# Optimization experiments

Hardware: AMD Instinct MI355X
Metric: run time of the kernel (lower is better)

Reference implementation:

```python
import jax, jax.numpy as jnp
import numpy as np

H = 256          # h_dim
SEQ_LEN = 10     # max history length
B = 2048         # number of queries with non-empty history
N = 327680       # total flattened neighbors across all (query, timestep) segments
NUM_SEG = B * SEQ_LEN
NUM_ENT = 20000
NUM_REL = 200


def setup_inputs() -> dict:
    key = jax.random.key(0)
    ks = jax.random.split(key, 9)
    s = jax.random.randint(ks[0], (B,), 0, NUM_ENT)
    r = jax.random.randint(ks[1], (B,), 0, NUM_REL)
    nbr_ids = jax.random.randint(ks[2], (N,), 0, NUM_ENT)
    seg_ids = jnp.sort(jax.random.randint(ks[3], (N,), 0, NUM_SEG))
    ent_embeds = jax.random.normal(ks[4], (NUM_ENT, H), dtype=jnp.float32)
    rel_embeds = jax.random.normal(ks[5], (NUM_REL, H), dtype=jnp.float32)
    W_attn = jax.random.normal(ks[6], (3 * H, H), dtype=jnp.float32) * 0.05
    b_attn = jax.random.normal(ks[7], (H,), dtype=jnp.float32) * 0.05
    v_s = jax.random.normal(ks[8], (H, 1), dtype=jnp.float32) * 0.05
    return {"s": s, "r": r, "nbr_ids": nbr_ids, "seg_ids": seg_ids,
            "ent_embeds": ent_embeds, "rel_embeds": rel_embeds,
            "W_attn": W_attn, "b_attn": b_attn, "v_s": v_s}


def reference(s, r, nbr_ids, seg_ids, ent_embeds, rel_embeds, W_attn, b_attn, v_s):
    # Per-neighbor gathers. Each neighbor belongs to segment seg = q*SEQ_LEN + t.
    q = seg_ids // SEQ_LEN                              # query index per neighbor [N]
    em = ent_embeds[nbr_ids]                            # [N, H] neighbor embeddings
    s_emb = ent_embeds[s]                               # [B, H]
    r_emb = rel_embeds[r]                               # [B, H]
    ss = s_emb[q]                                       # [N, H]
    rr = r_emb[q]                                       # [N, H]
    # Score: tanh(Linear(3H -> H)) @ v_s  -> scalar per neighbor
    x = jnp.concatenate([em, ss, rr], axis=1)           # [N, 3H]
    scores = (jnp.tanh(x @ W_attn + b_attn) @ v_s)[:, 0]  # [N]
    # Segment softmax over neighbors within each (query, timestep) segment.
    m = jax.ops.segment_max(scores, seg_ids, num_segments=NUM_SEG)  # [S]
    e = jnp.exp(scores - m[seg_ids])                    # [N]
    denom = jax.ops.segment_sum(e, seg_ids, num_segments=NUM_SEG)   # [S]
    w = e / denom[seg_ids]                              # [N]
    # Weighted sum of neighbor embeddings per segment (scatter-reduce).
    agg = jax.ops.segment_sum(w[:, None] * em, seg_ids, num_segments=NUM_SEG)  # [S, H]
    counts = jax.ops.segment_sum(jnp.ones_like(scores), seg_ids, num_segments=NUM_SEG)
    mask = (counts > 0).astype(em.dtype).reshape(B, SEQ_LEN, 1)     # present timesteps
    agg = agg.reshape(B, SEQ_LEN, H)
    ss_t = jnp.broadcast_to(s_emb[:, None, :], (B, SEQ_LEN, H))
    rr_t = jnp.broadcast_to(r_emb[:, None, :], (B, SEQ_LEN, H))
    # Padded [B, SEQ_LEN, 3H] sequence tensor (rows for empty segments are zero,
    # matching the torch code's zero-initialized padded tensor). Dropout p=0.0.
    out = jnp.concatenate([agg, ss_t, rr_t], axis=2) * mask
    return out
```

## Files before the change

kernel.cpp:

```cpp
#include <hip/hip_runtime.h>
#include <hip/hip_bf16.h>

#define H 256
#define SEQ 10
#define C2LOG2E 2.8853900817779268f
#define LOG2E 1.4426950408889634f

typedef __attribute__((ext_vector_type(8))) short bf16x8;
typedef __attribute__((ext_vector_type(4))) float f32x4;

__device__ __forceinline__ unsigned short f2bf(float x) {
    union { float f; unsigned u; } v; v.f = x;
    unsigned r = v.u + 0x7fff + ((v.u >> 16) & 1);
    return (unsigned short)(r >> 16);
}
__device__ __forceinline__ float bf2f(unsigned short b) {
    union { unsigned u; float f; } v; v.u = ((unsigned)b) << 16;
    return v.f;
}
__device__ __forceinline__ float fexp2(float x) {
    return __builtin_amdgcn_exp2f(x);
}

__global__ void prep_kernel(const float* __restrict__ W,
                            unsigned short* __restrict__ Wt,
                            const int* __restrict__ seg_ids,
                            int* __restrict__ seg_start,
                            int nWt, int n, int num_seg) {
    if ((int)blockIdx.x < nWt) {
        int idx = blockIdx.x * 256 + threadIdx.x;
        if (idx >= H * 3 * H) return;
        int nn = idx / (3 * H), k = idx % (3 * H);
        Wt[idx] = f2bf(C2LOG2E * W[k * H + nn]);
    } else {
        int j = (blockIdx.x - nWt) * 256 + threadIdx.x;
        if (j >= n) return;
        int cur = seg_ids[j];
        int prev = (j == 0) ? -1 : seg_ids[j - 1];
        for (int s2 = prev + 1; s2 <= cur; s2++) seg_start[s2] = j;
        if (j == n - 1)
            for (int s2 = cur + 1; s2 <= num_seg; s2++) seg_start[s2] = n;
    }
}

__global__ void gemm_bf16_kernel(const float* __restrict__ entf,
                                 const int* __restrict__ sidx,
                                 const int* __restrict__ ridx,
                                 const float* __restrict__ ent,
                                 const float* __restrict__ rel,
                                 const unsigned short* __restrict__ Wt,
                                 const float* __restrict__ bias,
                                 unsigned short* __restrict__ out,
                                 unsigned short* __restrict__ em_out,
                                 int M, int K, int k0, int mode, int ldo) {
    __shared__ unsigned short As[64][40];
    __shared__ unsigned short Bs[256][40];
    int t = threadIdx.x;
    int m0 = blockIdx.x * 64;
    int sr = t >> 2;
    int sc = (t & 3) * 8;
    int wave = t >> 6, lane = t & 63;
    int lr = lane & 15, lg = lane >> 4;

    f32x4 acc[4][4];
#pragma unroll
    for (int i = 0; i < 4; i++)
#pragma unroll
        for (int jn = 0; jn < 4; jn++) acc[i][jn] = (f32x4){0.f, 0.f, 0.f, 0.f};

    for (int kk = 0; kk < K; kk += 32) {
        bf16x8 av = {};
        int gm = m0 + sr;
        if (gm < M) {
            const float* src;
            if (mode == 0) {
                src = entf + (size_t)gm * H + kk + sc;
            } else {
                int k = kk + sc;
                src = (k < H) ? (ent + (size_t)sidx[gm] * H + k)
                              : (rel + (size_t)ridx[gm] * H + (k - H));
            }
            float4 f0 = *reinterpret_cast<const float4*>(src);
            float4 f1 = *reinterpret_cast<const float4*>(src + 4);
            av[0] = (short)f2bf(f0.x); av[1] = (short)f2bf(f0.y);
            av[2] = (short)f2bf(f0.z); av[3] = (short)f2bf(f0.w);
            av[4] = (short)f2bf(f1.x); av[5] = (short)f2bf(f1.y);
            av[6] = (short)f2bf(f1.z); av[7] = (short)f2bf(f1.w);
            if (mode == 0 && em_out)
                *reinterpret_cast<bf16x8*>(em_out + (size_t)gm * 512 + 256 + kk + sc) = av;
        }
        *reinterpret_cast<bf16x8*>(&As[sr][sc]) = av;
#pragma unroll
        for (int r4 = 0; r4 < 4; r4++) {
            int row = r4 * 64 + sr;
            bf16x8 bv = *reinterpret_cast<const bf16x8*>(
                Wt + (size_t)row * (3 * H) + k0 + kk + sc);
            *reinterpret_cast<bf16x8*>(&Bs[row][sc]) = bv;
        }
        __syncthreads();

        bf16x8 afr[4], bfr[4];
#pragma unroll
        for (int am = 0; am < 4; am++)
            afr[am] = *reinterpret_cast<const bf16x8*>(&As[am * 16 + lr][lg * 8]);
#pragma unroll
        for (int bn = 0; bn < 4; bn++)
            bfr[bn] = *reinterpret_cast<const bf16x8*>(&Bs[wave * 64 + bn * 16 + lr][lg * 8]);
#pragma unroll
        for (int am = 0; am < 4; am++)
#pragma unroll
            for (int bn = 0; bn < 4; bn++)
                acc[am][bn] = __builtin_amdgcn_mfma_f32_16x16x32_bf16(
                    afr[am], bfr[bn], acc[am][bn], 0, 0, 0);
        __syncthreads();
    }

#pragma unroll
    for (int bn = 0; bn < 4; bn++) {
        int col = wave * 64 + bn * 16 + lr;
        float bv = bias ? C2LOG2E * bias[col] : 0.f;
#pragma unroll
        for (int am = 0; am < 4; am++) {
#pragma unroll
            for (int rr = 0; rr < 4; rr++) {
                int row = m0 + am * 16 + lg * 4 + rr;
                if (row < M)
                    out[(size_t)row * ldo + col] = f2bf(acc[am][bn][rr] + bv);
            }
        }
    }
}

__global__ void __launch_bounds__(128, 4)
fused_agg_kernel(const int* __restrict__ nbr_ids,
                 const int* __restrict__ seg_start,
                 const unsigned short* __restrict__ comb,
                 const unsigned short* __restrict__ qpartbf,
                 const float* __restrict__ v_s,
                 const float* __restrict__ ent_embeds,
                 const float* __restrict__ rel_embeds,
                 const int* __restrict__ s,
                 const int* __restrict__ r,
                 float* __restrict__ out, int num_seg) {
    int wid = blockIdx.x * 2 + (threadIdx.x >> 6);
    int nw = gridDim.x * 2;
    int lane = threadIdx.x & 63;
    int g = lane >> 4, li = lane & 15;
    int cb = li * 16;
    int c4 = lane * 4;

    int chunk = (num_seg + nw - 1) / nw;
    int sbeg = wid * chunk;
    int send = min(sbeg + chunk, num_seg);

    float vm2[16];
    float vsum = 0.f;
    {
        const float4* vp = reinterpret_cast<const float4*>(v_s + cb);
#pragma unroll
        for (int k = 0; k < 4; k++) {
            float4 tv = vp[k];
            vm2[4 * k + 0] = -2.f * tv.x; vm2[4 * k + 1] = -2.f * tv.y;
            vm2[4 * k + 2] = -2.f * tv.z; vm2[4 * k + 3] = -2.f * tv.w;
            vsum += tv.x + tv.y + tv.z + tv.w;
        }
    }

    float qv[16];
    int bcur = -1;

    for (int seg = sbeg; seg < send; seg++) {
        int start = seg_start[seg], end = seg_start[seg + 1];
        int b = seg / SEQ;
        float* orow = out + (size_t)seg * (3 * H);

        if (start == end) {
            float4 z = {0.f, 0.f, 0.f, 0.f};
            *reinterpret_cast<float4*>(orow + c4) = z;
            *reinterpret_cast<float4*>(orow + H + c4) = z;
            *reinterpret_cast<float4*>(orow + 2 * H + c4) = z;
            continue;
        }

        if (b != bcur) {
            bcur = b;
            bf16x8 qa = *reinterpret_cast<const bf16x8*>(qpartbf + (size_t)b * H + cb);
            bf16x8 qb = *reinterpret_cast<const bf16x8*>(qpartbf + (size_t)b * H + cb + 8);
#pragma unroll
            for (int k = 0; k < 8; k++) {
                qv[k] = bf2f((unsigned short)qa[k]);
                qv[8 + k] = bf2f((unsigned short)qb[k]);
            }
        }

        float acc[16];
#pragma unroll
        for (int k = 0; k < 16; k++) acc[k] = 0.f;
        float lpart = 0.f;

        int cc = end - start;
        int nitm = (cc + 3) >> 2;

        int j0 = min(g, cc - 1);
        const unsigned short* row = comb + (size_t)nbr_ids[start + j0] * 512 + cb;
        bf16x8 p0 = *reinterpret_cast<const bf16x8*>(row);
        bf16x8 p1 = *reinterpret_cast<const bf16x8*>(row + 8);

        for (int ji = 0; ji < nitm; ji++) {
            bf16x8 e0 = *reinterpret_cast<const bf16x8*>(row + 256);
            bf16x8 e1 = *reinterpret_cast<const bf16x8*>(row + 264);
            int jn = min(4 * (ji + 1) + g, cc - 1);
            const unsigned short* rown = comb + (size_t)nbr_ids[start + jn] * 512 + cb;
            bf16x8 p0n = *reinterpret_cast<const bf16x8*>(rown);
            bf16x8 p1n = *reinterpret_cast<const bf16x8*>(rown + 8);

            float s16 = 0.f;
#pragma unroll
            for (int k = 0; k < 8; k++) {
                float r0 = __builtin_amdgcn_rcpf(
                    fexp2(bf2f((unsigned short)p0[k]) + qv[k]) + 1.f);
                s16 = fmaf(vm2[k], r0, s16);
                float r1 = __builtin_amdgcn_rcpf(
                    fexp2(bf2f((unsigned short)p1[k]) + qv[8 + k]) + 1.f);
                s16 = fmaf(vm2[8 + k], r1, s16);
            }
            s16 += vsum;
            s16 += __shfl_xor(s16, 1);
            s16 += __shfl_xor(s16, 2);
            s16 += __shfl_xor(s16, 4);
            s16 += __shfl_xor(s16, 8);
            float e = fexp2(s16 * LOG2E);
            e = (4 * ji + g < cc) ? e : 0.f;
            lpart += e;
#pragma unroll
            for (int k = 0; k < 8; k++) {
                acc[k] = fmaf(e, bf2f((unsigned short)e0[k]), acc[k]);
                acc[8 + k] = fmaf(e, bf2f((unsigned short)e1[k]), acc[8 + k]);
            }
            p0 = p0n; p1 = p1n; row = rown;
        }

        lpart += __shfl_xor(lpart, 16);
        lpart += __shfl_xor(lpart, 32);
#pragma unroll
        for (int k = 0; k < 16; k++) {
            acc[k] += __shfl_xor(acc[k], 16);
            acc[k] += __shfl_xor(acc[k], 32);
        }
        float invl = 1.f / lpart;

        float4 o;
#pragma unroll
        for (int k = 0; k < 4; k++) {
            float v0 = acc[k], v1 = acc[4 + k], v2 = acc[8 + k], v3 = acc[12 + k];
            float pick = (g == 0) ? v0 : (g == 1) ? v1 : (g == 2) ? v2 : v3;
            if (k == 0) o.x = pick * invl;
            else if (k == 1) o.y = pick * invl;
            else if (k == 2) o.z = pick * invl;
            else o.w = pick * invl;
        }
        *reinterpret_cast<float4*>(orow + cb + 4 * g) = o;
        *reinterpret_cast<float4*>(orow + H + c4) =
            *reinterpret_cast<const float4*>(ent_embeds + (size_t)s[b] * H + c4);
        *reinterpret_cast<float4*>(orow + 2 * H + c4) =
            *reinterpret_cast<const float4*>(rel_embeds + (size_t)r[b] * H + c4);
    }
}

extern "C" void kernel_launch(void* const* d_in, const int* in_sizes, int n_in,
                              void* d_out, int out_size, void* d_ws, size_t ws_size,
                              hipStream_t stream) {
    const int* s = (const int*)d_in[0];
    const int* r = (const int*)d_in[1];
    const int* nbr_ids = (const int*)d_in[2];
    const int* seg_ids = (const int*)d_in[3];
    const float* ent_embeds = (const float*)d_in[4];
    const float* rel_embeds = (const float*)d_in[5];
    const float* W_attn = (const float*)d_in[6];
    const float* b_attn = (const float*)d_in[7];
    const float* v_s = (const float*)d_in[8];
    float* out = (float*)d_out;

    int B = in_sizes[0];
    int N = in_sizes[2];
    int num_ent = in_sizes[4] / H;
    int num_seg = B * SEQ;

    char* ws = (char*)d_ws;
    unsigned short* comb = (unsigned short*)ws;
    unsigned short* Wt = comb + (size_t)num_ent * 512;
    unsigned short* qpartbf = Wt + (size_t)H * 3 * H;
    int* seg_start = (int*)(qpartbf + (size_t)B * H);

    int nWt = (H * 3 * H + 255) / 256;
    int nSeg = (N + 255) / 256;
    prep_kernel<<<nWt + nSeg, 256, 0, stream>>>(W_attn, Wt, seg_ids, seg_start,
                                                nWt, N, num_seg);

    gemm_bf16_kernel<<<(num_ent + 63) / 64, 256, 0, stream>>>(
        ent_embeds, nullptr, nullptr, nullptr, nullptr,
        Wt, nullptr, comb, comb, num_ent, H, 0, 0, 512);
    gemm_bf16_kernel<<<B / 64, 256, 0, stream>>>(
        nullptr, s, r, ent_embeds, rel_embeds,
        Wt, b_attn, qpartbf, nullptr, B, 2 * H, H, 1, H);

    fused_agg_kernel<<<2048, 128, 0, stream>>>(
        nbr_ids, seg_start, comb, qpartbf, v_s,
        ent_embeds, rel_embeds, s, r, out, num_seg);
}
```

Measured before the change: 106.0 us.

## Use atomic work-stealing for segment aggregation and merge the two GEMM launches

Static per-wave segment chunks in the aggregation kernel are replaced by dynamic work distribution, where each wave atomically grabs two segments from a global counter. This is meant to balance the uneven neighbor counts across segments. The entity-projection and query-projection GEMMs are merged into a single launch by splitting on block index, removing one kernel launch and letting the small query GEMM overlap with the larger one. Block size and launch bounds for the aggregation kernel also go up. The cost is atomic contention on one counter, and the counter has to be reset inside the prep kernel.

```diff
diff --git a/kernel.cpp b/kernel.cpp
--- a/kernel.cpp
+++ b/kernel.cpp
@@ -26,7 +26,9 @@
                             unsigned short* __restrict__ Wt,
                             const int* __restrict__ seg_ids,
                             int* __restrict__ seg_start,
+                            int* __restrict__ work_ctr,
                             int nWt, int n, int num_seg) {
+    if (blockIdx.x == 0 && threadIdx.x == 0) *work_ctr = 0;
     if ((int)blockIdx.x < nWt) {
         int idx = blockIdx.x * 256 + threadIdx.x;
         if (idx >= H * 3 * H) return;
@@ -46,17 +48,23 @@
 __global__ void gemm_bf16_kernel(const float* __restrict__ entf,
                                  const int* __restrict__ sidx,
                                  const int* __restrict__ ridx,
-                                 const float* __restrict__ ent,
                                  const float* __restrict__ rel,
                                  const unsigned short* __restrict__ Wt,
                                  const float* __restrict__ bias,
-                                 unsigned short* __restrict__ out,
-                                 unsigned short* __restrict__ em_out,
-                                 int M, int K, int k0, int mode, int ldo) {
+                                 unsigned short* __restrict__ comb,
+                                 unsigned short* __restrict__ qpart,
+                                 int nEntBlk, int M0, int M1) {
     __shared__ unsigned short As[64][40];
     __shared__ unsigned short Bs[256][40];
+    bool isEnt = (int)blockIdx.x < nEntBlk;
+    int m0 = (isEnt ? blockIdx.x : (blockIdx.x - nEntBlk)) * 64;
+    int M = isEnt ? M0 : M1;
+    int K = isEnt ? H : 2 * H;
+    int k0 = isEnt ? 0 : H;
+    int ldo = isEnt ? 512 : H;
+    unsigned short* outp = isEnt ? comb : qpart;
+
     int t = threadIdx.x;
-    int m0 = blockIdx.x * 64;
     int sr = t >> 2;
     int sc = (t & 3) * 8;
     int wave = t >> 6, lane = t & 63;
@@ -73,11 +81,11 @@
         int gm = m0 + sr;
         if (gm < M) {
             const float* src;
-            if (mode == 0) {
+            if (isEnt) {
                 src = entf + (size_t)gm * H + kk + sc;
             } else {
                 int k = kk + sc;
-                src = (k < H) ? (ent + (size_t)sidx[gm] * H + k)
+                src = (k < H) ? (entf + (size_t)sidx[gm] * H + k)
                               : (rel + (size_t)ridx[gm] * H + (k - H));
             }
             float4 f0 = *reinterpret_cast<const float4*>(src);
@@ -86,8 +94,8 @@
             av[2] = (short)f2bf(f0.z); av[3] = (short)f2bf(f0.w);
             av[4] = (short)f2bf(f1.x); av[5] = (short)f2bf(f1.y);
             av[6] = (short)f2bf(f1.z); av[7] = (short)f2bf(f1.w);
-            if (mode == 0 && em_out)
-                *reinterpret_cast<bf16x8*>(em_out + (size_t)gm * 512 + 256 + kk + sc) = av;
+            if (isEnt)
+                *reinterpret_cast<bf16x8*>(comb + (size_t)gm * 512 + 256 + kk + sc) = av;
         }
         *reinterpret_cast<bf16x8*>(&As[sr][sc]) = av;
 #pragma unroll
@@ -118,20 +126,20 @@
 #pragma unroll
     for (int bn = 0; bn < 4; bn++) {
         int col = wave * 64 + bn * 16 + lr;
-        float bv = bias ? C2LOG2E * bias[col] : 0.f;
+        float bv = isEnt ? 0.f : C2LOG2E * bias[col];
 #pragma unroll
         for (int am = 0; am < 4; am++) {
 #pragma unroll
             for (int rr = 0; rr < 4; rr++) {
                 int row = m0 + am * 16 + lg * 4 + rr;
                 if (row < M)
-                    out[(size_t)row * ldo + col] = f2bf(acc[am][bn][rr] + bv);
-            }
-        }
-    }
-}
-
-__global__ void __launch_bounds__(128, 4)
+                    outp[(size_t)row * ldo + col] = f2bf(acc[am][bn][rr] + bv);
+            }
+        }
+    }
+}
+
+__global__ void __launch_bounds__(256, 6)
 fused_agg_kernel(const int* __restrict__ nbr_ids,
                  const int* __restrict__ seg_start,
                  const unsigned short* __restrict__ comb,
@@ -141,17 +149,12 @@
                  const float* __restrict__ rel_embeds,
                  const int* __restrict__ s,
                  const int* __restrict__ r,
+                 int* __restrict__ work_ctr,
                  float* __restrict__ out, int num_seg) {
-    int wid = blockIdx.x * 2 + (threadIdx.x >> 6);
-    int nw = gridDim.x * 2;
     int lane = threadIdx.x & 63;
     int g = lane >> 4, li = lane & 15;
     int cb = li * 16;
     int c4 = lane * 4;
-
-    int chunk = (num_seg + nw - 1) / nw;
-    int sbeg = wid * chunk;
-    int send = min(sbeg + chunk, num_seg);
 
     float vm2[16];
     float vsum = 0.f;
@@ -169,101 +172,109 @@
     float qv[16];
     int bcur = -1;
 
-    for (int seg = sbeg; seg < send; seg++) {
-        int start = seg_start[seg], end = seg_start[seg + 1];
-        int b = seg / SEQ;
-        float* orow = out + (size_t)seg * (3 * H);
-
-        if (start == end) {
-            float4 z = {0.f, 0.f, 0.f, 0.f};
-            *reinterpret_cast<float4*>(orow + c4) = z;
-            *reinterpret_cast<float4*>(orow + H + c4) = z;
-            *reinterpret_cast<float4*>(orow + 2 * H + c4) = z;
-            continue;
-        }
-
-        if (b != bcur) {
-            bcur = b;
-            bf16x8 qa = *reinterpret_cast<const bf16x8*>(qpartbf + (size_t)b * H + cb);
-            bf16x8 qb = *reinterpret_cast<const bf16x8*>(qpartbf + (size_t)b * H + cb + 8);
-#pragma unroll
-            for (int k = 0; k < 8; k++) {
-                qv[k] = bf2f((unsigned short)qa[k]);
-                qv[8 + k] = bf2f((unsigned short)qb[k]);
-            }
-        }
-
-        float acc[16];
-#pragma unroll
-        for (int k = 0; k < 16; k++) acc[k] = 0.f;
-        float lpart = 0.f;
-
-        int cc = end - start;
-        int nitm = (cc + 3) >> 2;
-
-        int j0 = min(g, cc - 1);
-        const unsigned short* row = comb + (size_t)nbr_ids[start + j0] * 512 + cb;
-        bf16x8 p0 = *reinterpret_cast<const bf16x8*>(row);
-        bf16x8 p1 = *reinterpret_cast<const bf16x8*>(row + 8);
-
-        for (int ji = 0; ji < nitm; ji++) {
-            bf16x8 e0 = *reinterpret_cast<const bf16x8*>(row + 256);
-            bf16x8 e1 = *reinterpret_cast<const bf16x8*>(row + 264);
-            int jn = min(4 * (ji + 1) + g, cc - 1);
-            const unsigned short* rown = comb + (size_t)nbr_ids[start + jn] * 512 + cb;
-            bf16x8 p0n = *reinterpret_cast<const bf16x8*>(rown);
-            bf16x8 p1n = *reinterpret_cast<const bf16x8*>(rown + 8);
-
-            float s16 = 0.f;
-#pragma unroll
-            for (int k = 0; k < 8; k++) {
-                float r0 = __builtin_amdgcn_rcpf(
-                    fexp2(bf2f((unsigned short)p0[k]) + qv[k]) + 1.f);
-                s16 = fmaf(vm2[k], r0, s16);
-                float r1 = __builtin_amdgcn_rcpf(
-                    fexp2(bf2f((unsigned short)p1[k]) + qv[8 + k]) + 1.f);
-                s16 = fmaf(vm2[8 + k], r1, s16);
-            }
-            s16 += vsum;
-            s16 += __shfl_xor(s16, 1);
-            s16 += __shfl_xor(s16, 2);
-            s16 += __shfl_xor(s16, 4);
-            s16 += __shfl_xor(s16, 8);
-            float e = fexp2(s16 * LOG2E);
-            e = (4 * ji + g < cc) ? e : 0.f;
-            lpart += e;
-#pragma unroll
-            for (int k = 0; k < 8; k++) {
-                acc[k] = fmaf(e, bf2f((unsigned short)e0[k]), acc[k]);
-                acc[8 + k] = fmaf(e, bf2f((unsigned short)e1[k]), acc[8 + k]);
-            }
-            p0 = p0n; p1 = p1n; row = rown;
-        }
-
-        lpart += __shfl_xor(lpart, 16);
-        lpart += __shfl_xor(lpart, 32);
-#pragma unroll
-        for (int k = 0; k < 16; k++) {
-            acc[k] += __shfl_xor(acc[k], 16);
-            acc[k] += __shfl_xor(acc[k], 32);
-        }
-        float invl = 1.f / lpart;
-
-        float4 o;
-#pragma unroll
-        for (int k = 0; k < 4; k++) {
-            float v0 = acc[k], v1 = acc[4 + k], v2 = acc[8 + k], v3 = acc[12 + k];
-            float pick = (g == 0) ? v0 : (g == 1) ? v1 : (g == 2) ? v2 : v3;
-            if (k == 0) o.x = pick * invl;
-            else if (k == 1) o.y = pick * invl;
-            else if (k == 2) o.z = pick * invl;
-            else o.w = pick * invl;
-        }
-        *reinterpret_cast<float4*>(orow + cb + 4 * g) = o;
-        *reinterpret_cast<float4*>(orow + H + c4) =
-            *reinterpret_cast<const float4*>(ent_embeds + (size_t)s[b] * H + c4);
-        *reinterpret_cast<float4*>(orow + 2 * H + c4) =
-            *reinterpret_cast<const float4*>(rel_embeds + (size_t)r[b] * H + c4);
+    for (;;) {
+        int base = 0;
+        if (lane == 0) base = atomicAdd(work_ctr, 2);
+        base = __shfl(base, 0);
+        if (base >= num_seg) break;
+        int slim = min(base + 2, num_seg);
+
+        for (int seg = base; seg < slim; seg++) {
+            int start = seg_start[seg], end = seg_start[seg + 1];
+            int b = seg / SEQ;
+            float* orow = out + (size_t)seg * (3 * H);
+
+            if (start == end) {
+                float4 z = {0.f, 0.f, 0.f, 0.f};
+                *reinterpret_cast<float4*>(orow + c4) = z;
+                *reinterpret_cast<float4*>(orow + H + c4) = z;
+                *reinterpret_cast<float4*>(orow + 2 * H + c4) = z;
+                continue;
+            }
+
+            if (b != bcur) {
+                bcur = b;
+                bf16x8 qa = *reinterpret_cast<const bf16x8*>(qpartbf + (size_t)b * H + cb);
+                bf16x8 qb = *reinterpret_cast<const bf16x8*>(qpartbf + (size_t)b * H + cb + 8);
+#pragma unroll
+                for (int k = 0; k < 8; k++) {
+                    qv[k] = bf2f((unsigned short)qa[k]);
+                    qv[8 + k] = bf2f((unsigned short)qb[k]);
+                }
+            }
+
+            float acc[16];
+#pragma unroll
+            for (int k = 0; k < 16; k++) acc[k] = 0.f;
+            float lpart = 0.f;
+
+            int cc = end - start;
+            int nitm = (cc + 3) >> 2;
+
+            int j0 = min(g, cc - 1);
+            const unsigned short* row = comb + (size_t)nbr_ids[start + j0] * 512 + cb;
+            bf16x8 p0 = *reinterpret_cast<const bf16x8*>(row);
+            bf16x8 p1 = *reinterpret_cast<const bf16x8*>(row + 8);
+
+            for (int ji = 0; ji < nitm; ji++) {
+                bf16x8 e0 = *reinterpret_cast<const bf16x8*>(row + 256);
+                bf16x8 e1 = *reinterpret_cast<const bf16x8*>(row + 264);
+                int jn = min(4 * (ji + 1) + g, cc - 1);
+                const unsigned short* rown = comb + (size_t)nbr_ids[start + jn] * 512 + cb;
+                bf16x8 p0n = *reinterpret_cast<const bf16x8*>(rown);
+                bf16x8 p1n = *reinterpret_cast<const bf16x8*>(rown + 8);
+
+                float s16 = 0.f;
+#pragma unroll
+                for (int k = 0; k < 8; k++) {
+                    float r0 = __builtin_amdgcn_rcpf(
+                        fexp2(bf2f((unsigned short)p0[k]) + qv[k]) + 1.f);
+                    s16 = fmaf(vm2[k], r0, s16);
+                    float r1 = __builtin_amdgcn_rcpf(
+                        fexp2(bf2f((unsigned short)p1[k]) + qv[8 + k]) + 1.f);
+                    s16 = fmaf(vm2[8 + k], r1, s16);
+                }
+                s16 += vsum;
+                s16 += __shfl_xor(s16, 1);
+                s16 += __shfl_xor(s16, 2);
+                s16 += __shfl_xor(s16, 4);
+                s16 += __shfl_xor(s16, 8);
+                float e = fexp2(s16 * LOG2E);
+                e = (4 * ji + g < cc) ? e : 0.f;
+                lpart += e;
+#pragma unroll
+                for (int k = 0; k < 8; k++) {
+                    acc[k] = fmaf(e, bf2f((unsigned short)e0[k]), acc[k]);
+                    acc[8 + k] = fmaf(e, bf2f((unsigned short)e1[k]), acc[8 + k]);
+                }
+                p0 = p0n; p1 = p1n; row = rown;
+            }
+
+            lpart += __shfl_xor(lpart, 16);
+            lpart += __shfl_xor(lpart, 32);
+#pragma unroll
+            for (int k = 0; k < 16; k++) {
+                acc[k] += __shfl_xor(acc[k], 16);
+                acc[k] += __shfl_xor(acc[k], 32);
+            }
+            float invl = 1.f / lpart;
+
+            float4 o;
+#pragma unroll
+            for (int k = 0; k < 4; k++) {
+                float v0 = acc[k], v1 = acc[4 + k], v2 = acc[8 + k], v3 = acc[12 + k];
+                float pick = (g == 0) ? v0 : (g == 1) ? v1 : (g == 2) ? v2 : v3;
+                if (k == 0) o.x = pick * invl;
+                else if (k == 1) o.y = pick * invl;
+                else if (k == 2) o.z = pick * invl;
+                else o.w = pick * invl;
+            }
+            *reinterpret_cast<float4*>(orow + cb + 4 * g) = o;
+            *reinterpret_cast<float4*>(orow + H + c4) =
+                *reinterpret_cast<const float4*>(ent_embeds + (size_t)s[b] * H + c4);
+            *reinterpret_cast<float4*>(orow + 2 * H + c4) =
+                *reinterpret_cast<const float4*>(rel_embeds + (size_t)r[b] * H + c4);
+        }
     }
 }
 
@@ -291,20 +302,20 @@
     unsigned short* Wt = comb + (size_t)num_ent * 512;
     unsigned short* qpartbf = Wt + (size_t)H * 3 * H;
     int* seg_start = (int*)(qpartbf + (size_t)B * H);
+    int* work_ctr = seg_start + (num_seg + 1);
 
     int nWt = (H * 3 * H + 255) / 256;
     int nSeg = (N + 255) / 256;
     prep_kernel<<<nWt + nSeg, 256, 0, stream>>>(W_attn, Wt, seg_ids, seg_start,
-                                                nWt, N, num_seg);
-
-    gemm_bf16_kernel<<<(num_ent + 63) / 64, 256, 0, stream>>>(
-        ent_embeds, nullptr, nullptr, nullptr, nullptr,
-        Wt, nullptr, comb, comb, num_ent, H, 0, 0, 512);
-    gemm_bf16_kernel<<<B / 64, 256, 0, stream>>>(
-        nullptr, s, r, ent_embeds, rel_embeds,
-        Wt, b_attn, qpartbf, nullptr, B, 2 * H, H, 1, H);
-
-    fused_agg_kernel<<<2048, 128, 0, stream>>>(
+                                                work_ctr, nWt, N, num_seg);
+
+    int nEntBlk = (num_ent + 63) / 64;
+    int nQBlk = B / 64;
+    gemm_bf16_kernel<<<nEntBlk + nQBlk, 256, 0, stream>>>(
+        ent_embeds, s, r, rel_embeds, Wt, b_attn, comb, qpartbf,
+        nEntBlk, num_ent, B);
+
+    fused_agg_kernel<<<2048, 256, 0, stream>>>(
         nbr_ids, seg_start, comb, qpartbf, v_s,
-        ent_embeds, rel_embeds, s, r, out, num_seg);
-}
+        ent_embeds, rel_embeds, s, r, work_ctr, out, num_seg);
+}
```

Result: slower. 284.0 us (+168.0%).
